# Performance work log

Hardware: AMD Instinct MI355X
Metric: run time of the kernel (lower is better)

## Reference

```python
import jax, jax.numpy as jnp
import numpy as np

B, C, D, H, W = 1, 32, 48, 96, 192


def setup_inputs() -> dict:
    key = jax.random.key(0)
    ks = jax.random.split(key, 5)
    x = jax.random.normal(ks[0], (B, C, D, H, W), dtype=jnp.float32)
    gs = []
    for i in range(4):
        g = jax.random.uniform(ks[i + 1], (B, C, 5, H, W), dtype=jnp.float32)
        # GANet normalizes the 5 aggregation weights to sum to 1 per pixel
        g = g / jnp.sum(g, axis=2, keepdims=True)
        gs.append(g)
    return {"input": x, "g0": gs[0], "g1": gs[1], "g2": gs[2], "g3": gs[3]}


def _sga_dir(cost, g, axis, reverse):
    """Semi-global aggregation along one direction.

    cost: (B,C,D,H,W); g: (B,C,5,H,W). axis=4 scans along width, axis=3 along
    height; reverse flips the scan direction. Recurrence per step p:
      A(p,d) = w0*C(p,d) + w1*A(p-1,d) + w2*A(p-1,d-1) + w3*A(p-1,d+1)
               + w4*max_d' A(p-1,d')
    with A = C at the first position and d+-1 edge-clamped.
    """
    c = jnp.moveaxis(cost, axis, 0)  # (L, B, C, D, R)
    w = jnp.moveaxis(g, axis, 0)     # (L, B, C, 5, R)
    if reverse:
        c = c[::-1]
        w = w[::-1]

    def step(A, xs):
        cs, ws = xs  # cs: (B,C,D,R); ws: (B,C,5,R)
        w0, w1, w2, w3, w4 = (ws[:, :, k][:, :, None] for k in range(5))
        dm1 = jnp.concatenate([A[:, :, :1], A[:, :, :-1]], axis=2)  # d-1 (clamped)
        dp1 = jnp.concatenate([A[:, :, 1:], A[:, :, -1:]], axis=2)  # d+1 (clamped)
        mx = jnp.max(A, axis=2, keepdims=True)                      # max over d
        A_new = w0 * cs + w1 * A + w2 * dm1 + w3 * dp1 + w4 * mx
        return A_new, A_new

    A0 = c[0]
    _, outs = jax.lax.scan(step, A0, (c[1:], w[1:]))
    full = jnp.concatenate([A0[None], outs], axis=0)
    if reverse:
        full = full[::-1]
    return jnp.moveaxis(full, 0, axis)


def reference(input, g0, g1, g2, g3):
    a0 = _sga_dir(input, g0, 4, False)  # left -> right
    a1 = _sga_dir(input, g1, 4, True)   # right -> left
    a2 = _sga_dir(input, g2, 3, False)  # top -> bottom
    a3 = _sga_dir(input, g3, 3, True)   # bottom -> top
    # GANet selects the max over the 4 directions instead of summing
    return jnp.maximum(jnp.maximum(a0, a1), jnp.maximum(a2, a3))
```

## Files before the change

### kernel.cpp

```cpp
#include <hip/hip_runtime.h>

constexpr int Cc = 32;
constexpr int Dd = 48;
constexpr int Hh = 96;
constexpr int Ww = 192;
constexpr int TW = 16;
constexpr int NT = Ww / TW;
constexpr float NEGBIG = -3.402823466e+38f;

template <int CTRL, int RM>
__device__ __forceinline__ float dppmov(float v) {
    int i = __builtin_bit_cast(int, v);
    int r = __builtin_amdgcn_update_dpp(i, i, CTRL, RM, 0xF, false);
    return __builtin_bit_cast(float, r);
}

__device__ __forceinline__ float rdlane(float v, int idx) {
    int r = __builtin_amdgcn_readlane(__builtin_bit_cast(int, v), idx);
    return __builtin_bit_cast(float, r);
}

__device__ __forceinline__ unsigned f2h(float v) {
    return (unsigned)__builtin_bit_cast(unsigned short, (_Float16)v);
}
__device__ __forceinline__ float h2f(unsigned short u) {
    return (float)__builtin_bit_cast(_Float16, u);
}

__device__ __forceinline__ float wave_max48(float v) {
    v = fmaxf(v, dppmov<0x111, 0xF>(v));
    v = fmaxf(v, dppmov<0x112, 0xF>(v));
    v = fmaxf(v, dppmov<0x114, 0xF>(v));
    v = fmaxf(v, dppmov<0x118, 0xF>(v));
    v = fmaxf(v, dppmov<0x142, 0x2>(v));
    v = fmaxf(v, dppmov<0x143, 0x4>(v));
    return rdlane(v, 47);
}

__device__ __forceinline__ float sga_step(float A, float cs, float g0v, float g1v, float g2v,
                                          float g3v, float g4v, bool is47, bool first) {
    float dm1 = dppmov<0x138, 0xF>(A);
    float dp1 = dppmov<0x130, 0xF>(A);
    dp1 = is47 ? A : dp1;
    float mx = wave_max48(A);
    float r = g0v * cs + g1v * A + g2v * dm1 + g3v * dp1 + g4v * mx;
    return first ? cs : r;
}

template <bool WS>
__global__ __launch_bounds__(64, 4) void sga_w4(const float* __restrict__ x,
                                                const float* __restrict__ ga,
                                                const float* __restrict__ gb,
                                                float* __restrict__ out,
                                                const unsigned* __restrict__ ws) {
    __shared__ unsigned sstash[64][Dd];
    __shared__ float xo[Dd][TW + 1];

    const int bid = blockIdx.x;
    const int c = bid / Hh;
    const int h = bid - c * Hh;
    const int lane = threadIdx.x;
    const size_t HW = (size_t)Hh * Ww;

    const float* xrow = x + (size_t)c * Dd * HW + (size_t)h * Ww;
    const float* garow = ga + (size_t)c * 5 * HW + (size_t)h * Ww;
    const float* gbrow = gb + (size_t)c * 5 * HW + (size_t)h * Ww;
    float* orow = out + (size_t)c * Dd * HW + (size_t)h * Ww;
    const size_t wsrow = ((size_t)c * Hh + h) * Dd;

    const int dl = (lane < Dd) ? lane : (Dd - 1);
    const bool is47 = (lane == Dd - 1);

    int srow[3], scol[3];
#pragma unroll
    for (int i = 0; i < 3; ++i) {
        const int e4 = lane + i * 64;
        srow[i] = e4 >> 2;
        scol[i] = (e4 & 3) * 4;
    }
    const int gk = lane >> 4;
    const int gwi = lane & 15;

    float4 pre[3];
    float gA, g4r, gAn = 0.f, g4n = 0.f;
    unsigned tr[8];
    unsigned sv0[8], sv1[8], sv2[8], sv3[8];

    {
#pragma unroll
        for (int i = 0; i < 3; ++i)
            pre[i] = *reinterpret_cast<const float4*>(xrow + (size_t)srow[i] * HW + scol[i]);
        gA = garow[(size_t)gk * HW + gwi];
        g4r = garow[(size_t)4 * HW + gwi];
#pragma unroll
        for (int i = 0; i < 3; ++i) {
            xo[srow[i]][scol[i] + 0] = pre[i].x;
            xo[srow[i]][scol[i] + 1] = pre[i].y;
            xo[srow[i]][scol[i] + 2] = pre[i].z;
            xo[srow[i]][scol[i] + 3] = pre[i].w;
        }
    }

    float A = NEGBIG;

    for (int t = 0; t < NT; ++t) {
        if (t + 1 < NT) {
            const int wn = (t + 1) * TW;
#pragma unroll
            for (int i = 0; i < 3; ++i)
                pre[i] = *reinterpret_cast<const float4*>(xrow + (size_t)srow[i] * HW + wn + scol[i]);
            gAn = garow[(size_t)gk * HW + wn + gwi];
            g4n = garow[(size_t)4 * HW + wn + gwi];
        }
#pragma unroll
        for (int wk = 0; wk < TW; ++wk) {
            const float g0v = rdlane(gA, wk);
            const float g1v = rdlane(gA, 16 + wk);
            const float g2v = rdlane(gA, 32 + wk);
            const float g3v = rdlane(gA, 48 + wk);
            const float g4v = rdlane(g4r, wk);
            const float cs = xo[dl][wk];
            A = sga_step(A, cs, g0v, g1v, g2v, g3v, g4v, is47, (t == 0 && wk == 0));
            const unsigned hu = f2h(A);
            if ((wk & 1) == 0) tr[wk >> 1] = hu;
            else tr[wk >> 1] |= hu << 16;
        }
        if (t < 8) {
            if (lane < Dd) {
#pragma unroll
                for (int r = 0; r < 8; ++r) sstash[t * 8 + r][lane] = tr[r];
            }
        } else if (t == 8) {
#pragma unroll
            for (int r = 0; r < 8; ++r) sv0[r] = tr[r];
        } else if (t == 9) {
#pragma unroll
            for (int r = 0; r < 8; ++r) sv1[r] = tr[r];
        } else if (t == 10) {
#pragma unroll
            for (int r = 0; r < 8; ++r) sv2[r] = tr[r];
        } else {
#pragma unroll
            for (int r = 0; r < 8; ++r) sv3[r] = tr[r];
        }
        if (t + 1 < NT) {
#pragma unroll
            for (int i = 0; i < 3; ++i) {
                xo[srow[i]][scol[i] + 0] = pre[i].x;
                xo[srow[i]][scol[i] + 1] = pre[i].y;
                xo[srow[i]][scol[i] + 2] = pre[i].z;
                xo[srow[i]][scol[i] + 3] = pre[i].w;
            }
            gA = gAn;
            g4r = g4n;
        }
    }

    A = NEGBIG;
    unsigned wsc[6], wsn[6];
    {
        const int w0 = (NT - 1) * TW;
        gA = gbrow[(size_t)gk * HW + w0 + gwi];
        g4r = gbrow[(size_t)4 * HW + w0 + gwi];
        if constexpr (WS) {
#pragma unroll
            for (int i = 0; i < 3; ++i) {
                const size_t wb = (wsrow + srow[i]) * 96 + (w0 >> 1) + (scol[i] >> 1);
                wsc[2 * i] = ws[wb];
                wsc[2 * i + 1] = ws[wb + 1];
            }
        }
    }
    for (int t = NT - 1; t >= 0; --t) {
        const int w0 = t * TW;
        if (t > 0) {
            const int wn = w0 - TW;
#pragma unroll
            for (int i = 0; i < 3; ++i)
                pre[i] = *reinterpret_cast<const float4*>(xrow + (size_t)srow[i] * HW + wn + scol[i]);
            gAn = gbrow[(size_t)gk * HW + wn + gwi];
            g4n = gbrow[(size_t)4 * HW + wn + gwi];
            if constexpr (WS) {
#pragma unroll
                for (int i = 0; i < 3; ++i) {
                    const size_t wb = (wsrow + srow[i]) * 96 + (wn >> 1) + (scol[i] >> 1);
                    wsn[2 * i] = ws[wb];
                    wsn[2 * i + 1] = ws[wb + 1];
                }
            }
        }
        unsigned rr[8];
        if (t < 8) {
#pragma unroll
            for (int r = 0; r < 8; ++r) rr[r] = sstash[t * 8 + r][dl];
        } else if (t == 8) {
#pragma unroll
            for (int r = 0; r < 8; ++r) rr[r] = sv0[r];
        } else if (t == 9) {
#pragma unroll
            for (int r = 0; r < 8; ++r) rr[r] = sv1[r];
        } else if (t == 10) {
#pragma unroll
            for (int r = 0; r < 8; ++r) rr[r] = sv2[r];
        } else {
#pragma unroll
            for (int r = 0; r < 8; ++r) rr[r] = sv3[r];
        }
#pragma unroll
        for (int wk = TW - 1; wk >= 0; --wk) {
            const float g0v = rdlane(gA, wk);
            const float g1v = rdlane(gA, 16 + wk);
            const float g2v = rdlane(gA, 32 + wk);
            const float g3v = rdlane(gA, 48 + wk);
            const float g4v = rdlane(g4r, wk);
            const float cs = xo[dl][wk];
            A = sga_step(A, cs, g0v, g1v, g2v, g3v, g4v, is47, (t == NT - 1 && wk == TW - 1));
            const unsigned u = rr[wk >> 1];
            const float a0 = h2f((unsigned short)((wk & 1) ? (u >> 16) : (u & 0xffffu)));
            if (lane < Dd) xo[lane][wk] = fmaxf(A, a0);
        }
#pragma unroll
        for (int i = 0; i < 3; ++i) {
            float4 v;
            v.x = xo[srow[i]][scol[i] + 0];
            v.y = xo[srow[i]][scol[i] + 1];
            v.z = xo[srow[i]][scol[i] + 2];
            v.w = xo[srow[i]][scol[i] + 3];
            if constexpr (WS) {
                v.x = fmaxf(v.x, h2f((unsigned short)(wsc[2 * i] & 0xffffu)));
                v.y = fmaxf(v.y, h2f((unsigned short)(wsc[2 * i] >> 16)));
                v.z = fmaxf(v.z, h2f((unsigned short)(wsc[2 * i + 1] & 0xffffu)));
                v.w = fmaxf(v.w, h2f((unsigned short)(wsc[2 * i + 1] >> 16)));
            }
            *reinterpret_cast<float4*>(orow + (size_t)srow[i] * HW + w0 + scol[i]) = v;
        }
        if (t > 0) {
#pragma unroll
            for (int i = 0; i < 3; ++i) {
                xo[srow[i]][scol[i] + 0] = pre[i].x;
                xo[srow[i]][scol[i] + 1] = pre[i].y;
                xo[srow[i]][scol[i] + 2] = pre[i].z;
                xo[srow[i]][scol[i] + 3] = pre[i].w;
            }
#pragma unroll
            for (int i = 0; i < 6; ++i) wsc[i] = wsn[i];
            gA = gAn;
            g4r = g4n;
        }
    }
}

constexpr int WT2 = 4;
constexpr int KH2 = 4;
constexpr int NP2 = Hh / KH2;
constexpr int HALF = NP2 / 2;

template <bool WS>
__global__ __launch_bounds__(512, 2) void sga_h5(const float* __restrict__ x,
                                                 const float* __restrict__ gf,
                                                 const float* __restrict__ gr,
                                                 float* __restrict__ out,
                                                 unsigned* __restrict__ ws) {
    __shared__ unsigned short stash[WT2][2][Hh / 2][Dd];
    __shared__ float xs[2][2][KH2][Dd][WT2 + 1];
    __shared__ unsigned short osb[2][2][KH2][Dd][6];
    __shared__ float gs[2][2][KH2][WT2][8];

    const int xcd = blockIdx.x & 7;
    const int within = blockIdx.x >> 3;
    const int L = xcd * 192 + within;
    const int quad = L >> 2, sub = L & 3;
    const int c = quad / 12;
    const int wq = quad % 12;
    const int w0 = wq * 16 + sub * 4;

    const int tid = threadIdx.x;
    const int lane = tid & 63;
    const int wv = tid >> 6;
    const int col = wv >> 1;
    const int dir = wv & 1;
    const size_t HW = (size_t)Hh * Ww;

    const float* xb = x + (size_t)c * Dd * HW;
    const float* gfb = gf + (size_t)c * 5 * HW;
    const float* grb = gr + (size_t)c * 5 * HW;
    float* ob = out + (size_t)c * Dd * HW;

    const int dl = (lane < Dd) ? lane : (Dd - 1);
    const bool is47 = (lane == Dd - 1);

    int w_[3], d_[3], hp_[3], cu_[3];
    size_t xoff_[3];
#pragma unroll
    for (int j = 0; j < 3; ++j) {
        const int idx = tid + j * 512;
        w_[j] = idx & 3;
        const int t = idx >> 2;
        d_[j] = t % Dd;
        const int t2 = t / Dd;
        hp_[j] = t2 & 3;
        cu_[j] = t2 >> 2;
        xoff_[j] = (size_t)d_[j] * HW + (w0 + w_[j]);
    }
    const int gw_ = tid & 3;
    const int gk_ = (tid >> 2) % 5;
    const int ghc = (tid >> 2) / 5;
    const int ghp_ = ghc & 3;
    const int gcu_ = ghc >> 2;
    const bool gst = tid < 160;
    int fu_[2], fd_[2], fhp_[2], fcu_[2];
    bool fval_[2];
#pragma unroll
    for (int j = 0; j < 2; ++j) {
        int idx = tid + j * 512;
        fval_[j] = idx < 768;
        if (idx >= 768) idx = 767;
        fu_[j] = idx & 1;
        const int t = idx >> 1;
        fd_[j] = t % Dd;
        const int r = t / Dd;
        fhp_[j] = r & 3;
        fcu_[j] = r >> 2;
    }

    auto hofs = [&](int cur, int P, int hp) -> int {
        const int p = P * KH2 + hp;
        return cur ? (Hh - 1 - p) : p;
    };

    float xr_[3], grg = 0.f;
    float orr[2][3];

    {
#pragma unroll
        for (int j = 0; j < 3; ++j) xr_[j] = xb[xoff_[j] + (size_t)hofs(cu_[j], 0, hp_[j]) * Ww];
        if (gst) {
            const float* gp = gcu_ ? grb : gfb;
            grg = gp[(size_t)gk_ * HW + (size_t)hofs(gcu_, 0, ghp_) * Ww + (w0 + gw_)];
        }
#pragma unroll
        for (int j = 0; j < 3; ++j) xs[0][cu_[j]][hp_[j]][d_[j]][w_[j]] = xr_[j];
        if (gst) gs[0][gcu_][ghp_][gw_][gk_] = grg;
    }
    __syncthreads();

    float A = NEGBIG;

#pragma unroll 2
    for (int p = 0; p < NP2; ++p) {
        const int pb = p & 1;

        if (p + 1 < NP2) {
#pragma unroll
            for (int j = 0; j < 3; ++j)
                xr_[j] = xb[xoff_[j] + (size_t)hofs(cu_[j], p + 1, hp_[j]) * Ww];
            if (gst) {
                const float* gp = gcu_ ? grb : gfb;
                grg = gp[(size_t)gk_ * HW + (size_t)hofs(gcu_, p + 1, ghp_) * Ww + (w0 + gw_)];
            }
        }
        if constexpr (!WS) {
            if (p >= HALF) {
#pragma unroll
                for (int j = 0; j < 3; ++j)
                    orr[pb][j] = ob[xoff_[j] + (size_t)hofs(cu_[j], p, hp_[j]) * Ww];
            }
        }

#pragma unroll
        for (int hp = 0; hp < KH2; ++hp) {
            const int q = p * KH2 + hp;
            const float cs = xs[pb][dir][hp][dl][col];
            const float* gbase = &gs[pb][dir][hp][col][0];
            const float4 g03 = *reinterpret_cast<const float4*>(gbase);
            const float g4 = gbase[4];
            A = sga_step(A, cs, g03.x, g03.y, g03.z, g03.w, g4, is47, q == 0);
            if (q < Hh / 2) {
                if (lane < Dd) stash[col][dir][q][lane] = (unsigned short)f2h(A);
            } else {
                const float s = h2f(stash[col][dir ^ 1][Hh - 1 - q][dl]);
                const float o = fmaxf(A, s);
                if (lane < Dd) osb[pb][dir][hp][lane][col] = (unsigned short)f2h(o);
            }
        }

        if (p > HALF) {
            if constexpr (WS) {
#pragma unroll
                for (int j = 0; j < 2; ++j) {
                    if (fval_[j]) {
                        const unsigned* op =
                            reinterpret_cast<const unsigned*>(&osb[pb ^ 1][fcu_[j]][fhp_[j]][fd_[j]][0]);
                        const unsigned v = op[fu_[j]];
                        const int hh = hofs(fcu_[j], p - 1, fhp_[j]);
                        ws[(((size_t)c * Hh + hh) * Dd + fd_[j]) * 96 + (w0 >> 1) + fu_[j]] = v;
                    }
                }
            } else {
#pragma unroll
                for (int j = 0; j < 3; ++j) {
                    const float v = fmaxf(h2f(osb[pb ^ 1][cu_[j]][hp_[j]][d_[j]][w_[j]]),
                                          orr[pb ^ 1][j]);
                    ob[xoff_[j] + (size_t)hofs(cu_[j], p - 1, hp_[j]) * Ww] = v;
                }
            }
        }

        if (p + 1 < NP2) {
#pragma unroll
            for (int j = 0; j < 3; ++j) xs[pb ^ 1][cu_[j]][hp_[j]][d_[j]][w_[j]] = xr_[j];
            if (gst) gs[pb ^ 1][gcu_][ghp_][gw_][gk_] = grg;
        }
        __syncthreads();
    }

    if constexpr (WS) {
#pragma unroll
        for (int j = 0; j < 2; ++j) {
            if (fval_[j]) {
                const unsigned* op =
                    reinterpret_cast<const unsigned*>(&osb[1][fcu_[j]][fhp_[j]][fd_[j]][0]);
                const unsigned v = op[fu_[j]];
                const int hh = hofs(fcu_[j], NP2 - 1, fhp_[j]);
                ws[(((size_t)c * Hh + hh) * Dd + fd_[j]) * 96 + (w0 >> 1) + fu_[j]] = v;
            }
        }
    } else {
#pragma unroll
        for (int j = 0; j < 3; ++j) {
            const float v = fmaxf(h2f(osb[1][cu_[j]][hp_[j]][d_[j]][w_[j]]), orr[1][j]);
            ob[xoff_[j] + (size_t)hofs(cu_[j], NP2 - 1, hp_[j]) * Ww] = v;
        }
    }
}

extern "C" void kernel_launch(void* const* d_in, const int* in_sizes, int n_in,
                              void* d_out, int out_size, void* d_ws, size_t ws_size,
                              hipStream_t stream) {
    const float* x  = (const float*)d_in[0];
    const float* g0 = (const float*)d_in[1];
    const float* g1 = (const float*)d_in[2];
    const float* g2 = (const float*)d_in[3];
    const float* g3 = (const float*)d_in[4];
    float* out = (float*)d_out;

    const size_t WSNEED = (size_t)Cc * Hh * Dd * Ww * 2;
    if (ws_size >= WSNEED) {
        sga_h5<true><<<Cc * (Ww / (WT2 * 4)) * 4, 512, 0, stream>>>(x, g2, g3, out, (unsigned*)d_ws);
        sga_w4<true><<<Cc * Hh, 64, 0, stream>>>(x, g0, g1, out, (const unsigned*)d_ws);
    } else {
        sga_w4<false><<<Cc * Hh, 64, 0, stream>>>(x, g0, g1, out, nullptr);
        sga_h5<false><<<Cc * (Ww / (WT2 * 4)) * 4, 512, 0, stream>>>(x, g2, g3, out, nullptr);
    }
}
```

Measured before the change: 272.6 us.

## Drop fp16 workspace path; run width pass first, height pass merges via output

Removes the workspace-based path in which the height kernel wrote fp16 partial results to scratch for the width kernel to merge. Now the width kernel always runs first and writes fp32 output, and the height kernel reads that output back and takes the max. The output staging buffer moves from fp16 to fp32 in shared memory, and launch bounds rise to 4 blocks per SM. This trades the fp16 workspace write and read for an fp32 read of the output, and raises occupancy at the cost of register pressure.

```diff
diff --git a/kernel.cpp b/kernel.cpp
--- a/kernel.cpp
+++ b/kernel.cpp
@@ -47,12 +47,10 @@
     return first ? cs : r;
 }
 
-template <bool WS>
 __global__ __launch_bounds__(64, 4) void sga_w4(const float* __restrict__ x,
                                                 const float* __restrict__ ga,
                                                 const float* __restrict__ gb,
-                                                float* __restrict__ out,
-                                                const unsigned* __restrict__ ws) {
+                                                float* __restrict__ out) {
     __shared__ unsigned sstash[64][Dd];
     __shared__ float xo[Dd][TW + 1];
 
@@ -66,7 +64,6 @@
     const float* garow = ga + (size_t)c * 5 * HW + (size_t)h * Ww;
     const float* gbrow = gb + (size_t)c * 5 * HW + (size_t)h * Ww;
     float* orow = out + (size_t)c * Dd * HW + (size_t)h * Ww;
-    const size_t wsrow = ((size_t)c * Hh + h) * Dd;
 
     const int dl = (lane < Dd) ? lane : (Dd - 1);
     const bool is47 = (lane == Dd - 1);
@@ -157,19 +154,10 @@
     }
 
     A = NEGBIG;
-    unsigned wsc[6], wsn[6];
     {
         const int w0 = (NT - 1) * TW;
         gA = gbrow[(size_t)gk * HW + w0 + gwi];
         g4r = gbrow[(size_t)4 * HW + w0 + gwi];
-        if constexpr (WS) {
-#pragma unroll
-            for (int i = 0; i < 3; ++i) {
-                const size_t wb = (wsrow + srow[i]) * 96 + (w0 >> 1) + (scol[i] >> 1);
-                wsc[2 * i] = ws[wb];
-                wsc[2 * i + 1] = ws[wb + 1];
-            }
-        }
     }
     for (int t = NT - 1; t >= 0; --t) {
         const int w0 = t * TW;
@@ -180,14 +168,6 @@
                 pre[i] = *reinterpret_cast<const float4*>(xrow + (size_t)srow[i] * HW + wn + scol[i]);
             gAn = gbrow[(size_t)gk * HW + wn + gwi];
             g4n = gbrow[(size_t)4 * HW + wn + gwi];
-            if constexpr (WS) {
-#pragma unroll
-                for (int i = 0; i < 3; ++i) {
-                    const size_t wb = (wsrow + srow[i]) * 96 + (wn >> 1) + (scol[i] >> 1);
-                    wsn[2 * i] = ws[wb];
-                    wsn[2 * i + 1] = ws[wb + 1];
-                }
-            }
         }
         unsigned rr[8];
         if (t < 8) {
@@ -226,12 +206,6 @@
             v.y = xo[srow[i]][scol[i] + 1];
             v.z = xo[srow[i]][scol[i] + 2];
             v.w = xo[srow[i]][scol[i] + 3];
-            if constexpr (WS) {
-                v.x = fmaxf(v.x, h2f((unsigned short)(wsc[2 * i] & 0xffffu)));
-                v.y = fmaxf(v.y, h2f((unsigned short)(wsc[2 * i] >> 16)));
-                v.z = fmaxf(v.z, h2f((unsigned short)(wsc[2 * i + 1] & 0xffffu)));
-                v.w = fmaxf(v.w, h2f((unsigned short)(wsc[2 * i + 1] >> 16)));
-            }
             *reinterpret_cast<float4*>(orow + (size_t)srow[i] * HW + w0 + scol[i]) = v;
         }
         if (t > 0) {
@@ -242,8 +216,6 @@
                 xo[srow[i]][scol[i] + 2] = pre[i].z;
                 xo[srow[i]][scol[i] + 3] = pre[i].w;
             }
-#pragma unroll
-            for (int i = 0; i < 6; ++i) wsc[i] = wsn[i];
             gA = gAn;
             g4r = g4n;
         }
@@ -255,15 +227,13 @@
 constexpr int NP2 = Hh / KH2;
 constexpr int HALF = NP2 / 2;
 
-template <bool WS>
-__global__ __launch_bounds__(512, 2) void sga_h5(const float* __restrict__ x,
+__global__ __launch_bounds__(512, 4) void sga_h6(const float* __restrict__ x,
                                                  const float* __restrict__ gf,
                                                  const float* __restrict__ gr,
-                                                 float* __restrict__ out,
-                                                 unsigned* __restrict__ ws) {
-    __shared__ unsigned short stash[WT2][2][Hh / 2][Dd];
+                                                 float* __restrict__ out) {
+    __shared__ _Float16 stash[WT2][2][Hh / 2][Dd];
     __shared__ float xs[2][2][KH2][Dd][WT2 + 1];
-    __shared__ unsigned short osb[2][2][KH2][Dd][6];
+    __shared__ float osb[2][2][KH2][Dd][WT2 + 1];
     __shared__ float gs[2][2][KH2][WT2][8];
 
     const int xcd = blockIdx.x & 7;
@@ -308,28 +278,13 @@
     const int ghp_ = ghc & 3;
     const int gcu_ = ghc >> 2;
     const bool gst = tid < 160;
-    int fu_[2], fd_[2], fhp_[2], fcu_[2];
-    bool fval_[2];
-#pragma unroll
-    for (int j = 0; j < 2; ++j) {
-        int idx = tid + j * 512;
-        fval_[j] = idx < 768;
-        if (idx >= 768) idx = 767;
-        fu_[j] = idx & 1;
-        const int t = idx >> 1;
-        fd_[j] = t % Dd;
-        const int r = t / Dd;
-        fhp_[j] = r & 3;
-        fcu_[j] = r >> 2;
-    }
 
     auto hofs = [&](int cur, int P, int hp) -> int {
         const int p = P * KH2 + hp;
         return cur ? (Hh - 1 - p) : p;
     };
 
-    float xr_[3], grg = 0.f;
-    float orr[2][3];
+    float xr_[3], grg = 0.f, orr[2][3];
 
     {
 #pragma unroll
@@ -359,12 +314,10 @@
                 grg = gp[(size_t)gk_ * HW + (size_t)hofs(gcu_, p + 1, ghp_) * Ww + (w0 + gw_)];
             }
         }
-        if constexpr (!WS) {
-            if (p >= HALF) {
-#pragma unroll
-                for (int j = 0; j < 3; ++j)
-                    orr[pb][j] = ob[xoff_[j] + (size_t)hofs(cu_[j], p, hp_[j]) * Ww];
-            }
+        if (p >= HALF) {
+#pragma unroll
+            for (int j = 0; j < 3; ++j)
+                orr[pb][j] = ob[xoff_[j] + (size_t)hofs(cu_[j], p, hp_[j]) * Ww];
         }
 
 #pragma unroll
@@ -376,33 +329,19 @@
             const float g4 = gbase[4];
             A = sga_step(A, cs, g03.x, g03.y, g03.z, g03.w, g4, is47, q == 0);
             if (q < Hh / 2) {
-                if (lane < Dd) stash[col][dir][q][lane] = (unsigned short)f2h(A);
+                if (lane < Dd) stash[col][dir][q][lane] = (_Float16)A;
             } else {
-                const float s = h2f(stash[col][dir ^ 1][Hh - 1 - q][dl]);
+                const float s = (float)stash[col][dir ^ 1][Hh - 1 - q][dl];
                 const float o = fmaxf(A, s);
-                if (lane < Dd) osb[pb][dir][hp][lane][col] = (unsigned short)f2h(o);
+                if (lane < Dd) osb[pb][dir][hp][lane][col] = o;
             }
         }
 
         if (p > HALF) {
-            if constexpr (WS) {
-#pragma unroll
-                for (int j = 0; j < 2; ++j) {
-                    if (fval_[j]) {
-                        const unsigned* op =
-                            reinterpret_cast<const unsigned*>(&osb[pb ^ 1][fcu_[j]][fhp_[j]][fd_[j]][0]);
-                        const unsigned v = op[fu_[j]];
-                        const int hh = hofs(fcu_[j], p - 1, fhp_[j]);
-                        ws[(((size_t)c * Hh + hh) * Dd + fd_[j]) * 96 + (w0 >> 1) + fu_[j]] = v;
-                    }
-                }
-            } else {
-#pragma unroll
-                for (int j = 0; j < 3; ++j) {
-                    const float v = fmaxf(h2f(osb[pb ^ 1][cu_[j]][hp_[j]][d_[j]][w_[j]]),
-                                          orr[pb ^ 1][j]);
-                    ob[xoff_[j] + (size_t)hofs(cu_[j], p - 1, hp_[j]) * Ww] = v;
-                }
+#pragma unroll
+            for (int j = 0; j < 3; ++j) {
+                const float v = fmaxf(osb[pb ^ 1][cu_[j]][hp_[j]][d_[j]][w_[j]], orr[pb ^ 1][j]);
+                ob[xoff_[j] + (size_t)hofs(cu_[j], p - 1, hp_[j]) * Ww] = v;
             }
         }
 
@@ -414,21 +353,10 @@
         __syncthreads();
     }
 
-    if constexpr (WS) {
-#pragma unroll
-        for (int j = 0; j < 2; ++j) {
-            if (fval_[j]) {
-                const unsigned* op =
-                    reinterpret_cast<const unsigned*>(&osb[1][fcu_[j]][fhp_[j]][fd_[j]][0]);
-                const unsigned v = op[fu_[j]];
-                const int hh = hofs(fcu_[j], NP2 - 1, fhp_[j]);
-                ws[(((size_t)c * Hh + hh) * Dd + fd_[j]) * 96 + (w0 >> 1) + fu_[j]] = v;
-            }
-        }
-    } else {
+    {
 #pragma unroll
         for (int j = 0; j < 3; ++j) {
-            const float v = fmaxf(h2f(osb[1][cu_[j]][hp_[j]][d_[j]][w_[j]]), orr[1][j]);
+            const float v = fmaxf(osb[1][cu_[j]][hp_[j]][d_[j]][w_[j]], orr[1][j]);
             ob[xoff_[j] + (size_t)hofs(cu_[j], NP2 - 1, hp_[j]) * Ww] = v;
         }
     }
@@ -444,12 +372,6 @@
     const float* g3 = (const float*)d_in[4];
     float* out = (float*)d_out;
 
-    const size_t WSNEED = (size_t)Cc * Hh * Dd * Ww * 2;
-    if (ws_size >= WSNEED) {
-        sga_h5<true><<<Cc * (Ww / (WT2 * 4)) * 4, 512, 0, stream>>>(x, g2, g3, out, (unsigned*)d_ws);
-        sga_w4<true><<<Cc * Hh, 64, 0, stream>>>(x, g0, g1, out, (const unsigned*)d_ws);
-    } else {
-        sga_w4<false><<<Cc * Hh, 64, 0, stream>>>(x, g0, g1, out, nullptr);
-        sga_h5<false><<<Cc * (Ww / (WT2 * 4)) * 4, 512, 0, stream>>>(x, g2, g3, out, nullptr);
-    }
-}
+    sga_w4<<<Cc * Hh, 64, 0, stream>>>(x, g0, g1, out);
+    sga_h6<<<Cc * (Ww / 16) * 4, 512, 0, stream>>>(x, g2, g3, out);
+}
```

Result: slower. 287.4 us (+5.4%).
